# Performance work log

Measured on AMD Instinct MI355X. Metric: run time of the kernel, lower is better.

The kernel has to match this reference:

```python
import jax, jax.numpy as jnp
import numpy as np

EPS = 1e-6  # flax LayerNorm default

def _layernorm(x, scale, bias):
    mu = jnp.mean(x, axis=-1, keepdims=True)
    var = jnp.mean(jnp.square(x - mu), axis=-1, keepdims=True)
    return (x - mu) * jax.lax.rsqrt(var + EPS) * scale + bias

def _rel_pos_index(ws):
    coords = np.stack(np.meshgrid(np.arange(ws), np.arange(ws), indexing='ij'))  # [2,ws,ws]
    cf = coords.reshape(2, -1)
    rel = (cf[:, :, None] - cf[:, None, :]).transpose(1, 2, 0)  # [N,N,2]
    rel[..., 0] += ws - 1
    rel[..., 1] += ws - 1
    rel[..., 0] *= 2 * ws - 1
    return rel.sum(-1)  # [N,N] in [0,(2ws-1)^2)

def setup_inputs() -> dict:
    key = jax.random.key(0)
    ks = jax.random.split(key, 8)
    B, H, W, C = 16, 56, 56, 384
    L, heads, ws = 2, 12, 7
    s = 0.02
    return {
        'x': jax.random.normal(ks[0], (B, H, W, C), jnp.float32),
        'ln1_s': jnp.ones((L, C), jnp.float32),
        'ln1_b': jnp.zeros((L, C), jnp.float32),
        'qkv_w': jax.random.normal(ks[1], (L, C, 3 * C), jnp.float32) * s,
        'rpb': jax.random.normal(ks[2], (L, (2 * ws - 1) ** 2, heads), jnp.float32) * s,
        'proj_w': jax.random.normal(ks[3], (L, C, C), jnp.float32) * s,
        'ln2_s': jnp.ones((L, C), jnp.float32),
        'ln2_b': jnp.zeros((L, C), jnp.float32),
        'mlp_w1': jax.random.normal(ks[4], (L, C, 4 * C), jnp.float32) * s,
        'mlp_b1': jnp.zeros((L, 4 * C), jnp.float32),
        'mlp_w2': jax.random.normal(ks[5], (L, 4 * C, C), jnp.float32) * s,
        'mlp_b2': jnp.zeros((L, C), jnp.float32),
        'window_size': 7,
    }

def reference(x, ln1_s, ln1_b, qkv_w, rpb, proj_w, ln2_s, ln2_b, mlp_w1, mlp_b1, mlp_w2, mlp_b2, window_size):
    B, H, W, C = x.shape
    ws = int(window_size)
    L = qkv_w.shape[0]
    heads = rpb.shape[-1]
    hd = C // heads
    N = ws * ws
    idx = jnp.asarray(_rel_pos_index(ws))  # [N,N] static

    # --- split to windows: [B,H,W,C] -> [B*nWh*nWw, N, C]
    xw = x.reshape(B, H // ws, ws, W // ws, ws, C)
    xw = xw.transpose(0, 1, 3, 2, 4, 5).reshape(-1, N, C)

    for l in range(L):
        # --- windowed MHSA with relative position bias
        h = _layernorm(xw, ln1_s[l], ln1_b[l])
        qkv = (h @ qkv_w[l]).reshape(-1, N, 3, heads, hd)
        q, k, v = qkv[:, :, 0], qkv[:, :, 1], qkv[:, :, 2]  # [nW,N,heads,hd]
        attn = jnp.einsum('wqhd,wkhd->whqk', q, k) * (hd ** -0.5)
        bias = rpb[l][idx].transpose(2, 0, 1)  # [heads,N,N]
        attn = jax.nn.softmax(attn + bias[None], axis=-1)
        o = jnp.einsum('whqk,wkhd->wqhd', attn, v).reshape(-1, N, C)
        xw = xw + o @ proj_w[l]
        # --- MLP block
        h = _layernorm(xw, ln2_s[l], ln2_b[l])
        h = jax.nn.gelu(h @ mlp_w1[l] + mlp_b1[l])
        xw = xw + (h @ mlp_w2[l] + mlp_b2[l])

    # --- merge windows back to [B,H,W,C]
    out = xw.reshape(B, H // ws, W // ws, ws, ws, C)
    out = out.transpose(0, 1, 3, 2, 4, 5).reshape(B, H, W, C)
    return out
```

## Files before the change

### kernel.cpp

```cpp
#include <hip/hip_runtime.h>
#include <hip/hip_bf16.h>

typedef __bf16 bf16;
typedef __attribute__((ext_vector_type(4))) __bf16 bf16x4;
typedef __attribute__((ext_vector_type(8))) __bf16 bf16x8;
typedef __attribute__((ext_vector_type(4))) float f32x4;

__device__ __forceinline__ void async_ld16(const void* g, void* l) {
    __builtin_amdgcn_global_load_lds(
        (const __attribute__((address_space(1))) unsigned int*)g,
        (__attribute__((address_space(3))) unsigned int*)l, 16, 0, 0);
}

__global__ __launch_bounds__(256) void k_f2bt(const float* __restrict__ in,
                                              bf16* __restrict__ out, int Kd, int Nd) {
    int id = blockIdx.x * 256 + threadIdx.x;
    if (id >= Kd * Nd) return;
    int k = id / Nd, n = id - k * Nd;
    out[(size_t)n * Kd + k] = (bf16)in[id];
}

__global__ __launch_bounds__(256) void k_lnr(const float* __restrict__ x,
                                             const float* __restrict__ s,
                                             const float* __restrict__ b,
                                             float* __restrict__ xres,
                                             bf16* __restrict__ h) {
    int traw = blockIdx.x * 4 + (threadIdx.x >> 6);
    int lane = threadIdx.x & 63;
    int bb = traw / 3136;
    int rem = traw - bb * 3136;
    int y = rem / 56, xc = rem - y * 56;
    int w = bb * 64 + (y / 7) * 8 + (xc / 7);
    int n = (y % 7) * 7 + (xc % 7);
    int twin = w * 49 + n;

    const float4* row = (const float4*)(x + (size_t)traw * 384);
    float4 v0 = row[lane];
    float4 v1 = make_float4(0.f, 0.f, 0.f, 0.f);
    if (lane < 32) v1 = row[64 + lane];
    float sum = v0.x + v0.y + v0.z + v0.w + v1.x + v1.y + v1.z + v1.w;
#pragma unroll
    for (int m = 1; m < 64; m <<= 1) sum += __shfl_xor(sum, m);
    float mu = sum * (1.f / 384.f);
    float sq = (v0.x - mu) * (v0.x - mu) + (v0.y - mu) * (v0.y - mu) +
               (v0.z - mu) * (v0.z - mu) + (v0.w - mu) * (v0.w - mu);
    if (lane < 32)
        sq += (v1.x - mu) * (v1.x - mu) + (v1.y - mu) * (v1.y - mu) +
              (v1.z - mu) * (v1.z - mu) + (v1.w - mu) * (v1.w - mu);
#pragma unroll
    for (int m = 1; m < 64; m <<= 1) sq += __shfl_xor(sq, m);
    float r = rsqrtf(sq * (1.f / 384.f) + 1e-6f);

    float4* xr = (float4*)(xres + (size_t)twin * 384);
    const float4* s4 = (const float4*)s;
    const float4* b4 = (const float4*)b;
    bf16* ho = h + (size_t)twin * 384;
    {
        xr[lane] = v0;
        float4 sv = s4[lane], bv = b4[lane];
        bf16x4 ov;
        ov[0] = (bf16)((v0.x - mu) * r * sv.x + bv.x);
        ov[1] = (bf16)((v0.y - mu) * r * sv.y + bv.y);
        ov[2] = (bf16)((v0.z - mu) * r * sv.z + bv.z);
        ov[3] = (bf16)((v0.w - mu) * r * sv.w + bv.w);
        *(bf16x4*)&ho[lane * 4] = ov;
    }
    if (lane < 32) {
        xr[64 + lane] = v1;
        float4 sv = s4[64 + lane], bv = b4[64 + lane];
        bf16x4 ov;
        ov[0] = (bf16)((v1.x - mu) * r * sv.x + bv.x);
        ov[1] = (bf16)((v1.y - mu) * r * sv.y + bv.y);
        ov[2] = (bf16)((v1.z - mu) * r * sv.z + bv.z);
        ov[3] = (bf16)((v1.w - mu) * r * sv.w + bv.w);
        *(bf16x4*)&ho[256 + lane * 4] = ov;
    }
}

__global__ __launch_bounds__(256) void k_ln(const float* __restrict__ xres,
                                            const float* __restrict__ s,
                                            const float* __restrict__ b,
                                            bf16* __restrict__ h) {
    int t = blockIdx.x * 4 + (threadIdx.x >> 6);
    int lane = threadIdx.x & 63;
    const float4* row = (const float4*)(xres + (size_t)t * 384);
    float4 v0 = row[lane];
    float4 v1 = make_float4(0.f, 0.f, 0.f, 0.f);
    if (lane < 32) v1 = row[64 + lane];
    float sum = v0.x + v0.y + v0.z + v0.w + v1.x + v1.y + v1.z + v1.w;
#pragma unroll
    for (int m = 1; m < 64; m <<= 1) sum += __shfl_xor(sum, m);
    float mu = sum * (1.f / 384.f);
    float sq = (v0.x - mu) * (v0.x - mu) + (v0.y - mu) * (v0.y - mu) +
               (v0.z - mu) * (v0.z - mu) + (v0.w - mu) * (v0.w - mu);
    if (lane < 32)
        sq += (v1.x - mu) * (v1.x - mu) + (v1.y - mu) * (v1.y - mu) +
              (v1.z - mu) * (v1.z - mu) + (v1.w - mu) * (v1.w - mu);
#pragma unroll
    for (int m = 1; m < 64; m <<= 1) sq += __shfl_xor(sq, m);
    float r = rsqrtf(sq * (1.f / 384.f) + 1e-6f);
    const float4* s4 = (const float4*)s;
    const float4* b4 = (const float4*)b;
    bf16* ho = h + (size_t)t * 384;
    {
        float4 sv = s4[lane], bv = b4[lane];
        bf16x4 ov;
        ov[0] = (bf16)((v0.x - mu) * r * sv.x + bv.x);
        ov[1] = (bf16)((v0.y - mu) * r * sv.y + bv.y);
        ov[2] = (bf16)((v0.z - mu) * r * sv.z + bv.z);
        ov[3] = (bf16)((v0.w - mu) * r * sv.w + bv.w);
        *(bf16x4*)&ho[lane * 4] = ov;
    }
    if (lane < 32) {
        float4 sv = s4[64 + lane], bv = b4[64 + lane];
        bf16x4 ov;
        ov[0] = (bf16)((v1.x - mu) * r * sv.x + bv.x);
        ov[1] = (bf16)((v1.y - mu) * r * sv.y + bv.y);
        ov[2] = (bf16)((v1.z - mu) * r * sv.z + bv.z);
        ov[3] = (bf16)((v1.w - mu) * r * sv.w + bv.w);
        *(bf16x4*)&ho[256 + lane * 4] = ov;
    }
}

__device__ inline float gelu_f(float x) {
    float u = 0.7978845608028654f * (x + 0.044715f * x * x * x);
    float t = 1.f - 2.f / (__expf(2.f * u) + 1.f);
    return 0.5f * x * (1.f + t);
}

template <int EPI>
__global__ __launch_bounds__(256) void k_gemm(const bf16* __restrict__ A,
                                              const bf16* __restrict__ Bt,
                                              const float* __restrict__ bias,
                                              float* __restrict__ resid,
                                              bf16* __restrict__ Cout,
                                              float* __restrict__ outf,
                                              int N, int K) {
    __shared__ __align__(16) char lds[49152];
    int tid = threadIdx.x;

    int nwg = gridDim.x * gridDim.y;
    int orig = blockIdx.y * gridDim.x + blockIdx.x;
    int q = nwg >> 3, r8 = nwg & 7;
    int xcd = orig & 7, idx = orig >> 3;
    int wg = (xcd < r8 ? xcd * (q + 1) : r8 * (q + 1) + (xcd - r8) * q) + idx;
    int n0 = (wg % gridDim.x) * 128;
    int m0 = (wg / gridDim.x) * 128;

    int wave = tid >> 6, lane = tid & 63;
    int wm = (wave >> 1) * 64, wn = (wave & 1) * 64;
    int col = lane & 15, quad = lane >> 4;

    f32x4 acc[4][4] = {};

    int r0 = 2 * wave * 16 + (lane >> 2);
    int ksl = (lane & 3) ^ ((r0 >> 1) & 3);
    const bf16* ga0 = A + (size_t)(m0 + r0) * K + ksl * 8;
    const bf16* gb0 = Bt + (size_t)(n0 + r0) * K + ksl * 8;
    size_t rowK16 = (size_t)16 * K;
    int ldsoff = 2 * wave * 512;

    int NT = K >> 5;

    auto stage = [&](int t, int b) {
        const bf16* a = ga0 + t * 32;
        const bf16* g = gb0 + t * 32;
        char* base = (char*)lds + b * 16384;
        bf16* Ab = (bf16*)base;
        bf16* Bb = (bf16*)(base + 8192);
        async_ld16(a, Ab + ldsoff);
        async_ld16(a + rowK16, Ab + ldsoff + 512);
        async_ld16(g, Bb + ldsoff);
        async_ld16(g + rowK16, Bb + ldsoff + 512);
    };

    stage(0, 0);
    stage(1, 1);

    int buf = 0;
    for (int t = 0; t < NT; ++t) {
        if (t < NT - 1)
            asm volatile("s_waitcnt vmcnt(4) lgkmcnt(0)\n\ts_barrier" ::: "memory");
        else
            asm volatile("s_waitcnt vmcnt(0) lgkmcnt(0)\n\ts_barrier" ::: "memory");

        if (t + 2 < NT) {
            int sb = buf + 2; if (sb >= 3) sb -= 3;
            stage(t + 2, sb);
        }

        const char* base = (const char*)lds + buf * 16384;
        const bf16* Ab = (const bf16*)base;
        const bf16* Bb = (const bf16*)(base + 8192);
        bf16x8 af[4], bfv[4];
#pragma unroll
        for (int i = 0; i < 4; i++) {
            int ra = wm + i * 16 + col;
            af[i] = *(const bf16x8*)&Ab[ra * 32 + ((quad ^ ((ra >> 1) & 3)) << 3)];
            int rb = wn + i * 16 + col;
            bfv[i] = *(const bf16x8*)&Bb[rb * 32 + ((quad ^ ((rb >> 1) & 3)) << 3)];
        }
#pragma unroll
        for (int mi = 0; mi < 4; mi++)
#pragma unroll
            for (int ni = 0; ni < 4; ni++)
                acc[mi][ni] = __builtin_amdgcn_mfma_f32_16x16x32_bf16(
                    af[mi], bfv[ni], acc[mi][ni], 0, 0, 0);
        buf = (buf == 2) ? 0 : buf + 1;
    }

    __syncthreads();
    float* scrw = (float*)lds + wave * (16 * 68);

    int prow = lane >> 3;
    int pc0 = (lane & 7) * 8;
#pragma unroll
    for (int mi = 0; mi < 4; mi++) {
#pragma unroll
        for (int ni = 0; ni < 4; ni++)
#pragma unroll
            for (int r = 0; r < 4; r++)
                scrw[(quad * 4 + r) * 68 + ni * 16 + col] = acc[mi][ni][r];
#pragma unroll
        for (int h = 0; h < 2; h++) {
            int lr = h * 8 + prow;
            const float* sp = scrw + lr * 68 + pc0;
            float4 u0 = *(const float4*)sp;
            float4 u1 = *(const float4*)(sp + 4);
            int gm = m0 + wm + mi * 16 + lr;
            int gn = n0 + wn + pc0;
            size_t off = (size_t)gm * N + gn;
            if (EPI == 0) {
                bf16x8 ov;
                ov[0] = (bf16)u0.x; ov[1] = (bf16)u0.y; ov[2] = (bf16)u0.z; ov[3] = (bf16)u0.w;
                ov[4] = (bf16)u1.x; ov[5] = (bf16)u1.y; ov[6] = (bf16)u1.z; ov[7] = (bf16)u1.w;
                *(bf16x8*)&Cout[off] = ov;
            } else if (EPI == 1) {
                float4 b0 = *(const float4*)&bias[gn];
                float4 b1 = *(const float4*)&bias[gn + 4];
                bf16x8 ov;
                ov[0] = (bf16)gelu_f(u0.x + b0.x); ov[1] = (bf16)gelu_f(u0.y + b0.y);
                ov[2] = (bf16)gelu_f(u0.z + b0.z); ov[3] = (bf16)gelu_f(u0.w + b0.w);
                ov[4] = (bf16)gelu_f(u1.x + b1.x); ov[5] = (bf16)gelu_f(u1.y + b1.y);
                ov[6] = (bf16)gelu_f(u1.z + b1.z); ov[7] = (bf16)gelu_f(u1.w + b1.w);
                *(bf16x8*)&Cout[off] = ov;
            } else if (EPI == 2) {
                float4 r0v = *(const float4*)&resid[off];
                float4 r1v = *(const float4*)&resid[off + 4];
                r0v.x += u0.x; r0v.y += u0.y; r0v.z += u0.z; r0v.w += u0.w;
                r1v.x += u1.x; r1v.y += u1.y; r1v.z += u1.z; r1v.w += u1.w;
                *(float4*)&resid[off] = r0v;
                *(float4*)&resid[off + 4] = r1v;
            } else if (EPI == 3) {
                float4 b0 = *(const float4*)&bias[gn];
                float4 b1 = *(const float4*)&bias[gn + 4];
                float4 r0v = *(const float4*)&resid[off];
                float4 r1v = *(const float4*)&resid[off + 4];
                r0v.x += u0.x + b0.x; r0v.y += u0.y + b0.y;
                r0v.z += u0.z + b0.z; r0v.w += u0.w + b0.w;
                r1v.x += u1.x + b1.x; r1v.y += u1.y + b1.y;
                r1v.z += u1.z + b1.z; r1v.w += u1.w + b1.w;
                *(float4*)&resid[off] = r0v;
                *(float4*)&resid[off + 4] = r1v;
            } else {
                float4 b0 = *(const float4*)&bias[gn];
                float4 b1 = *(const float4*)&bias[gn + 4];
                float4 r0v = *(const float4*)&resid[off];
                float4 r1v = *(const float4*)&resid[off + 4];
                r0v.x += u0.x + b0.x; r0v.y += u0.y + b0.y;
                r0v.z += u0.z + b0.z; r0v.w += u0.w + b0.w;
                r1v.x += u1.x + b1.x; r1v.y += u1.y + b1.y;
                r1v.z += u1.z + b1.z; r1v.w += u1.w + b1.w;
                int wdx = gm / 49, n = gm - wdx * 49;
                int bb = wdx >> 6, r64 = wdx & 63;
                int n7 = n / 7;
                int yy = (r64 >> 3) * 7 + n7;
                int xx = (r64 & 7) * 7 + (n - n7 * 7);
                size_t traw = ((size_t)((bb * 56 + yy) * 56 + xx)) * 384 + gn;
                *(float4*)&outf[traw] = r0v;
                *(float4*)&outf[traw + 4] = r1v;
            }
        }
    }
}

__global__ __launch_bounds__(256) void k_attn(const bf16* __restrict__ qkv,
                                              const float* __restrict__ rpb,
                                              bf16* __restrict__ o) {
    __shared__ unsigned short relIdx[2401];
    __shared__ float rpbs[4][169];
    __shared__ __align__(16) bf16 Vs[4][32 * 72];
    __shared__ __align__(16) bf16 Ps[4][64 * 72];

    int tid = threadIdx.x;
    int wave = tid >> 6, lane = tid & 63;
    int col = lane & 15, quad = lane >> 4;
    int w = blockIdx.x;
    int head = blockIdx.y * 4 + wave;
    const float scale = 0.17677669529663687f;

    for (int e = tid; e < 2401; e += 256) {
        int i = e / 49, j = e - i * 49;
        int yi = i / 7, xi = i - yi * 7, yj = j / 7, xj = j - yj * 7;
        relIdx[e] = (unsigned short)((yi - yj + 6) * 13 + (xi - xj + 6));
    }
    for (int e = lane; e < 169; e += 64) rpbs[wave][e] = rpb[e * 12 + head];

    const bf16* base = qkv + (size_t)w * 49 * 1152 + head * 32;
    bf16* vsw = Vs[wave];
    bf16* psw = Ps[wave];

    bf16x4 z4 = {(bf16)0.f, (bf16)0.f, (bf16)0.f, (bf16)0.f};
    for (int e = lane; e < 576; e += 64) *(bf16x4*)&vsw[e * 4] = z4;
    for (int e = lane; e < 392; e += 64) {
        int j = e >> 3, d4 = (e & 7) * 4;
        bf16x4 vv = *(const bf16x4*)&base[768 + (size_t)j * 1152 + d4];
        vsw[(d4 + 0) * 72 + j] = vv[0];
        vsw[(d4 + 1) * 72 + j] = vv[1];
        vsw[(d4 + 2) * 72 + j] = vv[2];
        vsw[(d4 + 3) * 72 + j] = vv[3];
    }

    __syncthreads();

    bf16x8 qf[4], kf[4];
#pragma unroll
    for (int mi = 0; mi < 4; mi++) {
        size_t row = (size_t)(mi * 16 + col) * 1152 + quad * 8;
        qf[mi] = *(const bf16x8*)&base[row];
        kf[mi] = *(const bf16x8*)&base[384 + row];
    }

    f32x4 S[4][4] = {};
#pragma unroll
    for (int mi = 0; mi < 4; mi++)
#pragma unroll
        for (int nj = 0; nj < 4; nj++)
            S[mi][nj] = __builtin_amdgcn_mfma_f32_16x16x32_bf16(qf[mi], kf[nj], S[mi][nj], 0, 0, 0);

    float* rp = rpbs[wave];
#pragma unroll
    for (int mi = 0; mi < 4; mi++) {
#pragma unroll
        for (int r = 0; r < 4; r++) {
            int ii = mi * 16 + quad * 4 + r;
            int ir = (ii < 49 ? ii : 0) * 49;
            float sv[4];
            float mx = -1e30f;
#pragma unroll
            for (int nj = 0; nj < 4; nj++) {
                int j = nj * 16 + col;
                float v;
                if (j < 49) v = S[mi][nj][r] * scale + rp[relIdx[ir + j]];
                else v = -1e30f;
                sv[nj] = v;
                mx = fmaxf(mx, v);
            }
#pragma unroll
            for (int m = 1; m < 16; m <<= 1) mx = fmaxf(mx, __shfl_xor(mx, m));
            float sum = 0.f;
#pragma unroll
            for (int nj = 0; nj < 4; nj++) {
                float p = __expf(sv[nj] - mx);
                sv[nj] = p;
                sum += p;
            }
#pragma unroll
            for (int m = 1; m < 16; m <<= 1) sum += __shfl_xor(sum, m);
            float is = 1.f / sum;
#pragma unroll
            for (int nj = 0; nj < 4; nj++)
                psw[ii * 72 + nj * 16 + col] = (bf16)(sv[nj] * is);
        }
    }

    __syncthreads();

    f32x4 O[4][2] = {};
#pragma unroll
    for (int kt = 0; kt < 2; kt++) {
        bf16x8 vb[2];
#pragma unroll
        for (int nt = 0; nt < 2; nt++)
            vb[nt] = *(const bf16x8*)&vsw[(nt * 16 + col) * 72 + kt * 32 + quad * 8];
#pragma unroll
        for (int mi = 0; mi < 4; mi++) {
            bf16x8 pa = *(const bf16x8*)&psw[(mi * 16 + col) * 72 + kt * 32 + quad * 8];
#pragma unroll
            for (int nt = 0; nt < 2; nt++)
                O[mi][nt] = __builtin_amdgcn_mfma_f32_16x16x32_bf16(pa, vb[nt], O[mi][nt], 0, 0, 0);
        }
    }

    bf16* ob = o + (size_t)w * 49 * 384 + head * 32;
#pragma unroll
    for (int mi = 0; mi < 4; mi++) {
#pragma unroll
        for (int r = 0; r < 4; r++) {
            int i = mi * 16 + quad * 4 + r;
            if (i < 49) {
#pragma unroll
                for (int nt = 0; nt < 2; nt++)
                    ob[(size_t)i * 384 + nt * 16 + col] = (bf16)O[mi][nt][r];
            }
        }
    }
}

extern "C" void kernel_launch(void* const* d_in, const int* in_sizes, int n_in,
                              void* d_out, int out_size, void* d_ws, size_t ws_size,
                              hipStream_t stream) {
    const float* x      = (const float*)d_in[0];
    const float* ln1_s  = (const float*)d_in[1];
    const float* ln1_b  = (const float*)d_in[2];
    const float* qkv_w  = (const float*)d_in[3];
    const float* rpb    = (const float*)d_in[4];
    const float* proj_w = (const float*)d_in[5];
    const float* ln2_s  = (const float*)d_in[6];
    const float* ln2_b  = (const float*)d_in[7];
    const float* mlp_w1 = (const float*)d_in[8];
    const float* mlp_b1 = (const float*)d_in[9];
    const float* mlp_w2 = (const float*)d_in[10];
    const float* mlp_b2 = (const float*)d_in[11];
    float* out = (float*)d_out;

    char* ws = (char*)d_ws;
    float* xres  = (float*)ws;
    bf16* qkvbuf = (bf16*)(ws + 77070336);
    bf16* obuf   = (bf16*)(ws + 192675840);
    bf16* wbuf   = (bf16*)(ws + 231211008);
    bf16* hidden = qkvbuf;
    bf16* hbuf   = (bf16*)d_out;

    bf16* qkvw_b  = wbuf;
    bf16* projw_b = wbuf + 884736;
    bf16* mlp1_b  = wbuf + 1179648;
    bf16* mlp2_b  = wbuf + 2359296;

    for (int l = 0; l < 2; l++) {
        k_f2bt<<<1728, 256, 0, stream>>>(qkv_w + (size_t)l * 442368,
                                         qkvw_b + (size_t)l * 442368, 384, 1152);
        k_f2bt<<<576, 256, 0, stream>>>(proj_w + (size_t)l * 147456,
                                        projw_b + (size_t)l * 147456, 384, 384);
        k_f2bt<<<2304, 256, 0, stream>>>(mlp_w1 + (size_t)l * 589824,
                                         mlp1_b + (size_t)l * 589824, 384, 1536);
        k_f2bt<<<2304, 256, 0, stream>>>(mlp_w2 + (size_t)l * 589824,
                                         mlp2_b + (size_t)l * 589824, 1536, 384);
    }

    k_lnr<<<12544, 256, 0, stream>>>(x, ln1_s, ln1_b, xres, hbuf);

    for (int l = 0; l < 2; l++) {
        k_gemm<0><<<dim3(9, 392), 256, 0, stream>>>(
            hbuf, qkvw_b + (size_t)l * 442368, nullptr, nullptr, qkvbuf, nullptr, 1152, 384);
        k_attn<<<dim3(1024, 3), 256, 0, stream>>>(qkvbuf, rpb + l * 2028, obuf);
        k_gemm<2><<<dim3(3, 392), 256, 0, stream>>>(
            obuf, projw_b + (size_t)l * 147456, nullptr, xres, nullptr, nullptr, 384, 384);
        k_ln<<<12544, 256, 0, stream>>>(xres, ln2_s + l * 384, ln2_b + l * 384, hbuf);
        k_gemm<1><<<dim3(12, 392), 256, 0, stream>>>(
            hbuf, mlp1_b + (size_t)l * 589824, mlp_b1 + l * 1536, nullptr, hidden, nullptr, 1536, 384);
        if (l == 0) {
            k_gemm<3><<<dim3(3, 392), 256, 0, stream>>>(
                hidden, mlp2_b, mlp_b2, xres, nullptr, nullptr, 384, 1536);
            k_ln<<<12544, 256, 0, stream>>>(xres, ln1_s + 384, ln1_b + 384, hbuf);
        } else {
            k_gemm<4><<<dim3(3, 392), 256, 0, stream>>>(
                hidden, mlp2_b + 589824, mlp_b2 + 384, xres, nullptr, out, 384, 1536);
        }
    }
}
```

Measured before the change: 1.084 ms.

## Process two M tiles per GEMM workgroup with double-buffered pipeline across tiles

Each GEMM workgroup now computes two consecutive 128-row M tiles, halving the grid, and prefetches the next tile's first K slice while the current tile finishes. That hides the pipeline fill between tiles. The LDS ring drops from three buffers to two with a full vmcnt(0) wait each step, and the epilogue scratch gets its own LDS region so it no longer conflicts with the staging buffers. The eight weight conversion launches are also merged into four using a layer grid dimension. The shallower prefetch and the halved grid (fewer workgroups per CU) may reduce latency hiding.

```diff
diff --git a/kernel.cpp b/kernel.cpp
--- a/kernel.cpp
+++ b/kernel.cpp
@@ -14,10 +14,11 @@
 
 __global__ __launch_bounds__(256) void k_f2bt(const float* __restrict__ in,
                                               bf16* __restrict__ out, int Kd, int Nd) {
+    size_t loff = (size_t)blockIdx.y * Kd * Nd;
     int id = blockIdx.x * 256 + threadIdx.x;
     if (id >= Kd * Nd) return;
     int k = id / Nd, n = id - k * Nd;
-    out[(size_t)n * Kd + k] = (bf16)in[id];
+    out[loff + (size_t)n * Kd + k] = (bf16)in[loff + id];
 }
 
 __global__ __launch_bounds__(256) void k_lnr(const float* __restrict__ x,
@@ -136,7 +137,7 @@
                                               bf16* __restrict__ Cout,
                                               float* __restrict__ outf,
                                               int N, int K) {
-    __shared__ __align__(16) char lds[49152];
+    __shared__ __align__(16) char lds[50176];
     int tid = threadIdx.x;
 
     int nwg = gridDim.x * gridDim.y;
@@ -145,140 +146,138 @@
     int xcd = orig & 7, idx = orig >> 3;
     int wg = (xcd < r8 ? xcd * (q + 1) : r8 * (q + 1) + (xcd - r8) * q) + idx;
     int n0 = (wg % gridDim.x) * 128;
-    int m0 = (wg / gridDim.x) * 128;
+    int mg = wg / gridDim.x;
 
     int wave = tid >> 6, lane = tid & 63;
     int wm = (wave >> 1) * 64, wn = (wave & 1) * 64;
     int col = lane & 15, quad = lane >> 4;
 
-    f32x4 acc[4][4] = {};
-
     int r0 = 2 * wave * 16 + (lane >> 2);
     int ksl = (lane & 3) ^ ((r0 >> 1) & 3);
-    const bf16* ga0 = A + (size_t)(m0 + r0) * K + ksl * 8;
-    const bf16* gb0 = Bt + (size_t)(n0 + r0) * K + ksl * 8;
+    const bf16* ga0 = A + ((size_t)mg * 256 + r0) * K + ksl * 8;
+    const bf16* gb0 = Bt + ((size_t)n0 + r0) * K + ksl * 8;
     size_t rowK16 = (size_t)16 * K;
+    size_t tileStride = (size_t)128 * K;
     int ldsoff = 2 * wave * 512;
 
     int NT = K >> 5;
 
-    auto stage = [&](int t, int b) {
-        const bf16* a = ga0 + t * 32;
-        const bf16* g = gb0 + t * 32;
+    auto stage = [&](int g, int t, int b) {
+        const bf16* a = ga0 + (size_t)g * tileStride + t * 32;
+        const bf16* gB = gb0 + t * 32;
         char* base = (char*)lds + b * 16384;
         bf16* Ab = (bf16*)base;
         bf16* Bb = (bf16*)(base + 8192);
         async_ld16(a, Ab + ldsoff);
         async_ld16(a + rowK16, Ab + ldsoff + 512);
-        async_ld16(g, Bb + ldsoff);
-        async_ld16(g + rowK16, Bb + ldsoff + 512);
+        async_ld16(gB, Bb + ldsoff);
+        async_ld16(gB + rowK16, Bb + ldsoff + 512);
     };
 
-    stage(0, 0);
-    stage(1, 1);
-
-    int buf = 0;
-    for (int t = 0; t < NT; ++t) {
-        if (t < NT - 1)
-            asm volatile("s_waitcnt vmcnt(4) lgkmcnt(0)\n\ts_barrier" ::: "memory");
-        else
-            asm volatile("s_waitcnt vmcnt(0) lgkmcnt(0)\n\ts_barrier" ::: "memory");
-
-        if (t + 2 < NT) {
-            int sb = buf + 2; if (sb >= 3) sb -= 3;
-            stage(t + 2, sb);
-        }
-
-        const char* base = (const char*)lds + buf * 16384;
-        const bf16* Ab = (const bf16*)base;
-        const bf16* Bb = (const bf16*)(base + 8192);
-        bf16x8 af[4], bfv[4];
-#pragma unroll
-        for (int i = 0; i < 4; i++) {
-            int ra = wm + i * 16 + col;
-            af[i] = *(const bf16x8*)&Ab[ra * 32 + ((quad ^ ((ra >> 1) & 3)) << 3)];
-            int rb = wn + i * 16 + col;
-            bfv[i] = *(const bf16x8*)&Bb[rb * 32 + ((quad ^ ((rb >> 1) & 3)) << 3)];
-        }
-#pragma unroll
-        for (int mi = 0; mi < 4; mi++)
-#pragma unroll
-            for (int ni = 0; ni < 4; ni++)
-                acc[mi][ni] = __builtin_amdgcn_mfma_f32_16x16x32_bf16(
-                    af[mi], bfv[ni], acc[mi][ni], 0, 0, 0);
-        buf = (buf == 2) ? 0 : buf + 1;
-    }
-
-    __syncthreads();
-    float* scrw = (float*)lds + wave * (16 * 68);
-
+    float* scrw = (float*)(lds + 32768) + wave * (16 * 68);
     int prow = lane >> 3;
     int pc0 = (lane & 7) * 8;
-#pragma unroll
-    for (int mi = 0; mi < 4; mi++) {
-#pragma unroll
-        for (int ni = 0; ni < 4; ni++)
-#pragma unroll
-            for (int r = 0; r < 4; r++)
-                scrw[(quad * 4 + r) * 68 + ni * 16 + col] = acc[mi][ni][r];
-#pragma unroll
-        for (int h = 0; h < 2; h++) {
-            int lr = h * 8 + prow;
-            const float* sp = scrw + lr * 68 + pc0;
-            float4 u0 = *(const float4*)sp;
-            float4 u1 = *(const float4*)(sp + 4);
-            int gm = m0 + wm + mi * 16 + lr;
-            int gn = n0 + wn + pc0;
-            size_t off = (size_t)gm * N + gn;
-            if (EPI == 0) {
-                bf16x8 ov;
-                ov[0] = (bf16)u0.x; ov[1] = (bf16)u0.y; ov[2] = (bf16)u0.z; ov[3] = (bf16)u0.w;
-                ov[4] = (bf16)u1.x; ov[5] = (bf16)u1.y; ov[6] = (bf16)u1.z; ov[7] = (bf16)u1.w;
-                *(bf16x8*)&Cout[off] = ov;
-            } else if (EPI == 1) {
-                float4 b0 = *(const float4*)&bias[gn];
-                float4 b1 = *(const float4*)&bias[gn + 4];
-                bf16x8 ov;
-                ov[0] = (bf16)gelu_f(u0.x + b0.x); ov[1] = (bf16)gelu_f(u0.y + b0.y);
-                ov[2] = (bf16)gelu_f(u0.z + b0.z); ov[3] = (bf16)gelu_f(u0.w + b0.w);
-                ov[4] = (bf16)gelu_f(u1.x + b1.x); ov[5] = (bf16)gelu_f(u1.y + b1.y);
-                ov[6] = (bf16)gelu_f(u1.z + b1.z); ov[7] = (bf16)gelu_f(u1.w + b1.w);
-                *(bf16x8*)&Cout[off] = ov;
-            } else if (EPI == 2) {
-                float4 r0v = *(const float4*)&resid[off];
-                float4 r1v = *(const float4*)&resid[off + 4];
-                r0v.x += u0.x; r0v.y += u0.y; r0v.z += u0.z; r0v.w += u0.w;
-                r1v.x += u1.x; r1v.y += u1.y; r1v.z += u1.z; r1v.w += u1.w;
-                *(float4*)&resid[off] = r0v;
-                *(float4*)&resid[off + 4] = r1v;
-            } else if (EPI == 3) {
-                float4 b0 = *(const float4*)&bias[gn];
-                float4 b1 = *(const float4*)&bias[gn + 4];
-                float4 r0v = *(const float4*)&resid[off];
-                float4 r1v = *(const float4*)&resid[off + 4];
-                r0v.x += u0.x + b0.x; r0v.y += u0.y + b0.y;
-                r0v.z += u0.z + b0.z; r0v.w += u0.w + b0.w;
-                r1v.x += u1.x + b1.x; r1v.y += u1.y + b1.y;
-                r1v.z += u1.z + b1.z; r1v.w += u1.w + b1.w;
-                *(float4*)&resid[off] = r0v;
-                *(float4*)&resid[off + 4] = r1v;
-            } else {
-                float4 b0 = *(const float4*)&bias[gn];
-                float4 b1 = *(const float4*)&bias[gn + 4];
-                float4 r0v = *(const float4*)&resid[off];
-                float4 r1v = *(const float4*)&resid[off + 4];
-                r0v.x += u0.x + b0.x; r0v.y += u0.y + b0.y;
-                r0v.z += u0.z + b0.z; r0v.w += u0.w + b0.w;
-                r1v.x += u1.x + b1.x; r1v.y += u1.y + b1.y;
-                r1v.z += u1.z + b1.z; r1v.w += u1.w + b1.w;
-                int wdx = gm / 49, n = gm - wdx * 49;
-                int bb = wdx >> 6, r64 = wdx & 63;
-                int n7 = n / 7;
-                int yy = (r64 >> 3) * 7 + n7;
-                int xx = (r64 & 7) * 7 + (n - n7 * 7);
-                size_t traw = ((size_t)((bb * 56 + yy) * 56 + xx)) * 384 + gn;
-                *(float4*)&outf[traw] = r0v;
-                *(float4*)&outf[traw + 4] = r1v;
+
+    stage(0, 0, 0);
+
+    for (int g = 0; g < 2; ++g) {
+        f32x4 acc[4][4] = {};
+        for (int t = 0; t < NT; ++t) {
+            int gt = g * NT + t;
+            asm volatile("s_waitcnt vmcnt(0) lgkmcnt(0)\n\ts_barrier" ::: "memory");
+
+            {
+                int t2 = t + 1, g2 = g;
+                if (t2 == NT) { t2 = 0; g2 = g + 1; }
+                if (g2 < 2) stage(g2, t2, (gt + 1) & 1);
+            }
+
+            const char* base = (const char*)lds + (gt & 1) * 16384;
+            const bf16* Ab = (const bf16*)base;
+            const bf16* Bb = (const bf16*)(base + 8192);
+            bf16x8 af[4], bfv[4];
+#pragma unroll
+            for (int i = 0; i < 4; i++) {
+                int ra = wm + i * 16 + col;
+                af[i] = *(const bf16x8*)&Ab[ra * 32 + ((quad ^ ((ra >> 1) & 3)) << 3)];
+                int rb = wn + i * 16 + col;
+                bfv[i] = *(const bf16x8*)&Bb[rb * 32 + ((quad ^ ((rb >> 1) & 3)) << 3)];
+            }
+#pragma unroll
+            for (int mi = 0; mi < 4; mi++)
+#pragma unroll
+                for (int ni = 0; ni < 4; ni++)
+                    acc[mi][ni] = __builtin_amdgcn_mfma_f32_16x16x32_bf16(
+                        af[mi], bfv[ni], acc[mi][ni], 0, 0, 0);
+        }
+
+        int m0g = (mg * 2 + g) * 128;
+#pragma unroll
+        for (int mi = 0; mi < 4; mi++) {
+#pragma unroll
+            for (int ni = 0; ni < 4; ni++)
+#pragma unroll
+                for (int r = 0; r < 4; r++)
+                    scrw[(quad * 4 + r) * 68 + ni * 16 + col] = acc[mi][ni][r];
+#pragma unroll
+            for (int h = 0; h < 2; h++) {
+                int lr = h * 8 + prow;
+                const float* sp = scrw + lr * 68 + pc0;
+                float4 u0 = *(const float4*)sp;
+                float4 u1 = *(const float4*)(sp + 4);
+                int gm = m0g + wm + mi * 16 + lr;
+                int gn = n0 + wn + pc0;
+                size_t off = (size_t)gm * N + gn;
+                if (EPI == 0) {
+                    bf16x8 ov;
+                    ov[0] = (bf16)u0.x; ov[1] = (bf16)u0.y; ov[2] = (bf16)u0.z; ov[3] = (bf16)u0.w;
+                    ov[4] = (bf16)u1.x; ov[5] = (bf16)u1.y; ov[6] = (bf16)u1.z; ov[7] = (bf16)u1.w;
+                    *(bf16x8*)&Cout[off] = ov;
+                } else if (EPI == 1) {
+                    float4 b0 = *(const float4*)&bias[gn];
+                    float4 b1 = *(const float4*)&bias[gn + 4];
+                    bf16x8 ov;
+                    ov[0] = (bf16)gelu_f(u0.x + b0.x); ov[1] = (bf16)gelu_f(u0.y + b0.y);
+                    ov[2] = (bf16)gelu_f(u0.z + b0.z); ov[3] = (bf16)gelu_f(u0.w + b0.w);
+                    ov[4] = (bf16)gelu_f(u1.x + b1.x); ov[5] = (bf16)gelu_f(u1.y + b1.y);
+                    ov[6] = (bf16)gelu_f(u1.z + b1.z); ov[7] = (bf16)gelu_f(u1.w + b1.w);
+                    *(bf16x8*)&Cout[off] = ov;
+                } else if (EPI == 2) {
+                    float4 r0v = *(const float4*)&resid[off];
+                    float4 r1v = *(const float4*)&resid[off + 4];
+                    r0v.x += u0.x; r0v.y += u0.y; r0v.z += u0.z; r0v.w += u0.w;
+                    r1v.x += u1.x; r1v.y += u1.y; r1v.z += u1.z; r1v.w += u1.w;
+                    *(float4*)&resid[off] = r0v;
+                    *(float4*)&resid[off + 4] = r1v;
+                } else if (EPI == 3) {
+                    float4 b0 = *(const float4*)&bias[gn];
+                    float4 b1 = *(const float4*)&bias[gn + 4];
+                    float4 r0v = *(const float4*)&resid[off];
+                    float4 r1v = *(const float4*)&resid[off + 4];
+                    r0v.x += u0.x + b0.x; r0v.y += u0.y + b0.y;
+                    r0v.z += u0.z + b0.z; r0v.w += u0.w + b0.w;
+                    r1v.x += u1.x + b1.x; r1v.y += u1.y + b1.y;
+                    r1v.z += u1.z + b1.z; r1v.w += u1.w + b1.w;
+                    *(float4*)&resid[off] = r0v;
+                    *(float4*)&resid[off + 4] = r1v;
+                } else {
+                    float4 b0 = *(const float4*)&bias[gn];
+                    float4 b1 = *(const float4*)&bias[gn + 4];
+                    float4 r0v = *(const float4*)&resid[off];
+                    float4 r1v = *(const float4*)&resid[off + 4];
+                    r0v.x += u0.x + b0.x; r0v.y += u0.y + b0.y;
+                    r0v.z += u0.z + b0.z; r0v.w += u0.w + b0.w;
+                    r1v.x += u1.x + b1.x; r1v.y += u1.y + b1.y;
+                    r1v.z += u1.z + b1.z; r1v.w += u1.w + b1.w;
+                    int wdx = gm / 49, n = gm - wdx * 49;
+                    int bb = wdx >> 6, r64 = wdx & 63;
+                    int n7 = n / 7;
+                    int yy = (r64 >> 3) * 7 + n7;
+                    int xx = (r64 & 7) * 7 + (n - n7 * 7);
+                    size_t traw = ((size_t)((bb * 56 + yy) * 56 + xx)) * 384 + gn;
+                    *(float4*)&outf[traw] = r0v;
+                    *(float4*)&outf[traw + 4] = r1v;
+                }
             }
         }
     }
@@ -437,34 +436,28 @@
     bf16* mlp1_b  = wbuf + 1179648;
     bf16* mlp2_b  = wbuf + 2359296;
 
+    k_f2bt<<<dim3(1728, 2), 256, 0, stream>>>(qkv_w, qkvw_b, 384, 1152);
+    k_f2bt<<<dim3(576, 2), 256, 0, stream>>>(proj_w, projw_b, 384, 384);
+    k_f2bt<<<dim3(2304, 2), 256, 0, stream>>>(mlp_w1, mlp1_b, 384, 1536);
+    k_f2bt<<<dim3(2304, 2), 256, 0, stream>>>(mlp_w2, mlp2_b, 1536, 384);
+
+    k_lnr<<<12544, 256, 0, stream>>>(x, ln1_s, ln1_b, xres, hbuf);
+
     for (int l = 0; l < 2; l++) {
-        k_f2bt<<<1728, 256, 0, stream>>>(qkv_w + (size_t)l * 442368,
-                                         qkvw_b + (size_t)l * 442368, 384, 1152);
-        k_f2bt<<<576, 256, 0, stream>>>(proj_w + (size_t)l * 147456,
-                                        projw_b + (size_t)l * 147456, 384, 384);
-        k_f2bt<<<2304, 256, 0, stream>>>(mlp_w1 + (size_t)l * 589824,
-                                         mlp1_b + (size_t)l * 589824, 384, 1536);
-        k_f2bt<<<2304, 256, 0, stream>>>(mlp_w2 + (size_t)l * 589824,
-                                         mlp2_b + (size_t)l * 589824, 1536, 384);
-    }
-
-    k_lnr<<<12544, 256, 0, stream>>>(x, ln1_s, ln1_b, xres, hbuf);
-
-    for (int l = 0; l < 2; l++) {
-        k_gemm<0><<<dim3(9, 392), 256, 0, stream>>>(
+        k_gemm<0><<<dim3(9, 196), 256, 0, stream>>>(
             hbuf, qkvw_b + (size_t)l * 442368, nullptr, nullptr, qkvbuf, nullptr, 1152, 384);
         k_attn<<<dim3(1024, 3), 256, 0, stream>>>(qkvbuf, rpb + l * 2028, obuf);
-        k_gemm<2><<<dim3(3, 392), 256, 0, stream>>>(
+        k_gemm<2><<<dim3(3, 196), 256, 0, stream>>>(
             obuf, projw_b + (size_t)l * 147456, nullptr, xres, nullptr, nullptr, 384, 384);
         k_ln<<<12544, 256, 0, stream>>>(xres, ln2_s + l * 384, ln2_b + l * 384, hbuf);
-        k_gemm<1><<<dim3(12, 392), 256, 0, stream>>>(
+        k_gemm<1><<<dim3(12, 196), 256, 0, stream>>>(
             hbuf, mlp1_b + (size_t)l * 589824, mlp_b1 + l * 1536, nullptr, hidden, nullptr, 1536, 384);
         if (l == 0) {
-            k_gemm<3><<<dim3(3, 392), 256, 0, stream>>>(
+            k_gemm<3><<<dim3(3, 196), 256, 0, stream>>>(
                 hidden, mlp2_b, mlp_b2, xres, nullptr, nullptr, 384, 1536);
             k_ln<<<12544, 256, 0, stream>>>(xres, ln1_s + 384, ln1_b + 384, hbuf);
         } else {
-            k_gemm<4><<<dim3(3, 392), 256, 0, stream>>>(
+            k_gemm<4><<<dim3(3, 196), 256, 0, stream>>>(
                 hidden, mlp2_b + 589824, mlp_b2 + 384, xres, nullptr, out, 384, 1536);
         }
     }
```

Result: slower. 1.172 ms (+8.1%).
